# Optimization experiments

Hardware: AMD Instinct MI355X
Metric: run time of the kernel (lower is better)

Reference implementation:

```python
import jax, jax.numpy as jnp
import numpy as np


def setup_inputs() -> dict:
    key = jax.random.key(0)
    k1, k2, k3, k4 = jax.random.split(key, 4)
    B, C_in, C_out, S = 128, 32, 8, 8192
    return {
        "x": jax.random.normal(k1, (B, C_in, S), dtype=jnp.float32),
        "w1": jax.random.normal(k2, (C_in, C_in, S), dtype=jnp.float32),
        "w2": jax.random.normal(k3, (C_out, C_in, S), dtype=jnp.float32),
        "bias": jax.random.normal(k4, (C_out, S), dtype=jnp.float32),
    }


def reference(x, w1, w2, bias):
    # Stage 1: (x.unsqueeze(1) * w1).sum(1) in torch sums the BROADCAST dim i,
    # so it reduces to an elementwise scale: out[b,j,s] = x[b,j,s] * sum_i w1[i,j,s]
    h = jnp.tanh(x * jnp.sum(w1, axis=0))            # (B, C_in, S)
    # Stage 2: true per-position contraction over the in-channel axis j
    out = jnp.einsum('bjs,ojs->bos', h, w2) + bias   # (B, C_out, S)
    return jnp.tanh(out)
```

## Files before the change

kernel.cpp:

```cpp
#include <hip/hip_runtime.h>
#include <cstddef>

#define SLEN 8192
#define CIN  32
#define COUT 8
#define BATCH 128
#define BCHUNK 4

__device__ __forceinline__ float fast_tanh(float x) {
    float t = __expf(2.0f * x);
    return 1.0f - 2.0f * __builtin_amdgcn_rcpf(t + 1.0f);
}

__global__ __launch_bounds__(256) void lc3_wsum(const float* __restrict__ w1,
                                                float* __restrict__ wsum) {
    int idx = blockIdx.x * 256 + threadIdx.x;
    int j   = idx / (SLEN / 4);
    int s4  = idx % (SLEN / 4);
    float4 acc = make_float4(0.f, 0.f, 0.f, 0.f);
    #pragma unroll
    for (int i = 0; i < CIN; ++i) {
        const float4 v = *reinterpret_cast<const float4*>(
            &w1[(size_t)(i * CIN + j) * SLEN + (size_t)s4 * 4]);
        acc.x += v.x; acc.y += v.y; acc.z += v.z; acc.w += v.w;
    }
    *reinterpret_cast<float4*>(&wsum[(size_t)j * SLEN + (size_t)s4 * 4]) = acc;
}

__global__ __launch_bounds__(256) void lc3_main(const float* __restrict__ x,
                                                const float* __restrict__ w1,
                                                const float* __restrict__ w2,
                                                const float* __restrict__ bias,
                                                const float* __restrict__ wsum,
                                                float* __restrict__ out,
                                                int have_ws) {
    const int s  = blockIdx.x * 256 + threadIdx.x;
    const int b0 = blockIdx.y * BCHUNK;

    float acc[BCHUNK][COUT];
    #pragma unroll
    for (int k = 0; k < BCHUNK; ++k)
        #pragma unroll
        for (int o = 0; o < COUT; ++o) acc[k][o] = 0.f;

    for (int j = 0; j < CIN; ++j) {
        float wsv;
        if (have_ws) {
            wsv = wsum[j * SLEN + s];
        } else {
            wsv = 0.f;
            #pragma unroll
            for (int i = 0; i < CIN; ++i) wsv += w1[(i * CIN + j) * SLEN + s];
        }
        float h[BCHUNK];
        #pragma unroll
        for (int k = 0; k < BCHUNK; ++k) {
            float xv = x[((b0 + k) * CIN + j) * SLEN + s];
            h[k] = fast_tanh(xv * wsv);
        }
        #pragma unroll
        for (int o = 0; o < COUT; ++o) {
            float wv = w2[(o * CIN + j) * SLEN + s];
            #pragma unroll
            for (int k = 0; k < BCHUNK; ++k)
                acc[k][o] = fmaf(h[k], wv, acc[k][o]);
        }
    }

    #pragma unroll
    for (int o = 0; o < COUT; ++o) {
        float bv = bias[o * SLEN + s];
        #pragma unroll
        for (int k = 0; k < BCHUNK; ++k)
            out[((b0 + k) * COUT + o) * SLEN + s] = fast_tanh(acc[k][o] + bv);
    }
}

extern "C" void kernel_launch(void* const* d_in, const int* in_sizes, int n_in,
                              void* d_out, int out_size, void* d_ws, size_t ws_size,
                              hipStream_t stream) {
    const float* x    = (const float*)d_in[0];
    const float* w1   = (const float*)d_in[1];
    const float* w2   = (const float*)d_in[2];
    const float* bias = (const float*)d_in[3];
    float* out  = (float*)d_out;
    float* wsum = (float*)d_ws;

    const size_t ws_needed = (size_t)CIN * SLEN * sizeof(float);
    const int have_ws = (ws_size >= ws_needed) ? 1 : 0;

    if (have_ws) {
        lc3_wsum<<<dim3(CIN * SLEN / 4 / 256), dim3(256), 0, stream>>>(w1, wsum);
    }

    dim3 grid(SLEN / 256, BATCH / BCHUNK);
    lc3_main<<<grid, dim3(256), 0, stream>>>(x, w1, w2, bias, wsum, out, have_ws);
}
```

Before: 43.56 us.

## Vectorize main kernel to two positions per thread and split wsum reduction

The main kernel now processes two adjacent sequence positions per thread using 2-wide vector loads, with nontemporal loads for x and nontemporal stores for out, and the grid is halved to match. The weight-sum kernel spreads the 32-way reduction over four warps per block with a shared-memory combine, giving it four times as many blocks. The fallback path that recomputed the weight sum inline when workspace was too small is removed, so the code now assumes a workspace is always provided. Wider per-thread work raises register use and halves the number of threads in the main kernel.

```diff
diff --git a/kernel.cpp b/kernel.cpp
--- a/kernel.cpp
+++ b/kernel.cpp
@@ -7,6 +7,9 @@
 #define BATCH 128
 #define BCHUNK 4
 
+typedef float v2f __attribute__((ext_vector_type(2)));
+typedef float v4f __attribute__((ext_vector_type(4)));
+
 __device__ __forceinline__ float fast_tanh(float x) {
     float t = __expf(2.0f * x);
     return 1.0f - 2.0f * __builtin_amdgcn_rcpf(t + 1.0f);
@@ -14,65 +17,74 @@
 
 __global__ __launch_bounds__(256) void lc3_wsum(const float* __restrict__ w1,
                                                 float* __restrict__ wsum) {
-    int idx = blockIdx.x * 256 + threadIdx.x;
-    int j   = idx / (SLEN / 4);
-    int s4  = idx % (SLEN / 4);
-    float4 acc = make_float4(0.f, 0.f, 0.f, 0.f);
+    __shared__ v4f part[4][64];
+    const int tx = threadIdx.x & 63;
+    const int ty = threadIdx.x >> 6;
+    const int g  = blockIdx.x * 64 + tx;
+    const int j  = g >> 11;
+    const int s4 = g & 2047;
+
+    v4f acc = (v4f)(0.f);
     #pragma unroll
-    for (int i = 0; i < CIN; ++i) {
-        const float4 v = *reinterpret_cast<const float4*>(
+    for (int ii = 0; ii < 8; ++ii) {
+        const int i = ty * 8 + ii;
+        acc += *reinterpret_cast<const v4f*>(
             &w1[(size_t)(i * CIN + j) * SLEN + (size_t)s4 * 4]);
-        acc.x += v.x; acc.y += v.y; acc.z += v.z; acc.w += v.w;
     }
-    *reinterpret_cast<float4*>(&wsum[(size_t)j * SLEN + (size_t)s4 * 4]) = acc;
+    part[ty][tx] = acc;
+    __syncthreads();
+    if (ty == 0) {
+        v4f r = part[0][tx] + part[1][tx] + part[2][tx] + part[3][tx];
+        *reinterpret_cast<v4f*>(&wsum[(size_t)j * SLEN + (size_t)s4 * 4]) = r;
+    }
 }
 
 __global__ __launch_bounds__(256) void lc3_main(const float* __restrict__ x,
-                                                const float* __restrict__ w1,
                                                 const float* __restrict__ w2,
                                                 const float* __restrict__ bias,
                                                 const float* __restrict__ wsum,
-                                                float* __restrict__ out,
-                                                int have_ws) {
-    const int s  = blockIdx.x * 256 + threadIdx.x;
+                                                float* __restrict__ out) {
+    const int s  = (blockIdx.x * 256 + threadIdx.x) * 2;
     const int b0 = blockIdx.y * BCHUNK;
 
-    float acc[BCHUNK][COUT];
+    v2f acc[BCHUNK][COUT];
     #pragma unroll
     for (int k = 0; k < BCHUNK; ++k)
         #pragma unroll
-        for (int o = 0; o < COUT; ++o) acc[k][o] = 0.f;
+        for (int o = 0; o < COUT; ++o) acc[k][o] = (v2f)(0.f);
 
     for (int j = 0; j < CIN; ++j) {
-        float wsv;
-        if (have_ws) {
-            wsv = wsum[j * SLEN + s];
-        } else {
-            wsv = 0.f;
-            #pragma unroll
-            for (int i = 0; i < CIN; ++i) wsv += w1[(i * CIN + j) * SLEN + s];
-        }
-        float h[BCHUNK];
+        const v2f wsv = *reinterpret_cast<const v2f*>(&wsum[j * SLEN + s]);
+        v2f h[BCHUNK];
         #pragma unroll
         for (int k = 0; k < BCHUNK; ++k) {
-            float xv = x[((b0 + k) * CIN + j) * SLEN + s];
-            h[k] = fast_tanh(xv * wsv);
+            const v2f xv = __builtin_nontemporal_load(
+                reinterpret_cast<const v2f*>(&x[((b0 + k) * CIN + j) * SLEN + s]));
+            h[k].x = fast_tanh(xv.x * wsv.x);
+            h[k].y = fast_tanh(xv.y * wsv.y);
         }
         #pragma unroll
         for (int o = 0; o < COUT; ++o) {
-            float wv = w2[(o * CIN + j) * SLEN + s];
+            const v2f wv = *reinterpret_cast<const v2f*>(&w2[(o * CIN + j) * SLEN + s]);
             #pragma unroll
-            for (int k = 0; k < BCHUNK; ++k)
-                acc[k][o] = fmaf(h[k], wv, acc[k][o]);
+            for (int k = 0; k < BCHUNK; ++k) {
+                acc[k][o].x = fmaf(h[k].x, wv.x, acc[k][o].x);
+                acc[k][o].y = fmaf(h[k].y, wv.y, acc[k][o].y);
+            }
         }
     }
 
     #pragma unroll
     for (int o = 0; o < COUT; ++o) {
-        float bv = bias[o * SLEN + s];
+        const v2f bv = *reinterpret_cast<const v2f*>(&bias[o * SLEN + s]);
         #pragma unroll
-        for (int k = 0; k < BCHUNK; ++k)
-            out[((b0 + k) * COUT + o) * SLEN + s] = fast_tanh(acc[k][o] + bv);
+        for (int k = 0; k < BCHUNK; ++k) {
+            v2f r;
+            r.x = fast_tanh(acc[k][o].x + bv.x);
+            r.y = fast_tanh(acc[k][o].y + bv.y);
+            __builtin_nontemporal_store(
+                r, reinterpret_cast<v2f*>(&out[((b0 + k) * COUT + o) * SLEN + s]));
+        }
     }
 }
 
@@ -86,13 +98,8 @@
     float* out  = (float*)d_out;
     float* wsum = (float*)d_ws;
 
-    const size_t ws_needed = (size_t)CIN * SLEN * sizeof(float);
-    const int have_ws = (ws_size >= ws_needed) ? 1 : 0;
+    lc3_wsum<<<dim3(CIN * SLEN / 4 / 64), dim3(256), 0, stream>>>(w1, wsum);
 
-    if (have_ws) {
-        lc3_wsum<<<dim3(CIN * SLEN / 4 / 256), dim3(256), 0, stream>>>(w1, wsum);
-    }
-
-    dim3 grid(SLEN / 256, BATCH / BCHUNK);
-    lc3_main<<<grid, dim3(256), 0, stream>>>(x, w1, w2, bias, wsum, out, have_ws);
+    dim3 grid(SLEN / 2 / 256, BATCH / BCHUNK);
+    lc3_main<<<grid, dim3(256), 0, stream>>>(x, w2, bias, wsum, out);
 }
```

Result: slower. 55.54 us (+27.5%).
